# Optimization experiments

Measured on AMD Instinct MI355X. Metric: run time of the kernel, lower is better.

Reference implementation:

```python
import jax, jax.numpy as jnp
import numpy as np

N = 2_097_152  # total atoms
G = 32_768     # number of graphs (~64 atoms each)
EPS = 1e-4     # sign-detection threshold from the original code


def setup_inputs() -> dict:
    key = jax.random.key(0)
    k1, k2 = jax.random.split(key)
    pos = jax.random.normal(k1, (N, 3), dtype=jnp.float32) * 3.0
    batch = jnp.sort(jax.random.randint(k2, (N,), 0, G))
    return {"pos": pos, "batch": batch, "num_graphs": G}


def reference(pos, batch, num_graphs):
    n = pos.shape[0]
    dtype = pos.dtype

    # per-graph centroid (scatter_mean)
    counts = jax.ops.segment_sum(jnp.ones((n,), dtype), batch, num_segments=num_graphs)
    center = jax.ops.segment_sum(pos, batch, num_segments=num_graphs) / jnp.maximum(counts, 1.0)[:, None]
    pc = pos - center[batch]                      # [N,3] centered positions

    # per-atom inertia contribution: r^2 * I - p p^T, then scatter_add per graph
    r_sq = jnp.sum(pc * pc, axis=-1)              # [N]
    outer = jnp.einsum('ni,nj->nij', pc, pc)      # [N,3,3]
    I_atom = r_sq[:, None, None] * jnp.eye(3, dtype=dtype) - outer
    I_mol = jax.ops.segment_sum(I_atom, batch, num_segments=num_graphs)  # [G,3,3]

    L, Q = jnp.linalg.eigh(I_mol)                 # Q: [G,3,3], columns = principal axes

    # projections of centered positions onto the (pre-flip) eigenbasis.
    # NOTE: in the torch loop, p_proj is computed once before any sign flips, and
    # flipping column 0 does not affect p_proj[:,1], so axes 0 and 1 are independent.
    proj = jnp.einsum('ni,nij->nj', pc, Q[batch])  # [N,3]

    idx = jnp.arange(n)

    def axis_sign(a):
        # parallel "first atom (in original order) with |proj| > EPS" per graph
        qual = jnp.abs(proj[:, a]) > EPS
        key_idx = jnp.where(qual, idx, n)
        first = jax.ops.segment_min(key_idx, batch, num_segments=num_graphs)  # [G]
        found = first < n
        val = proj[jnp.minimum(first, n - 1), a]
        return jnp.where(found & (val < 0), -1.0, 1.0).astype(dtype)

    s0 = axis_sign(0)
    s1 = axis_sign(1)
    q0 = Q[:, :, 0] * s0[:, None]
    q1 = Q[:, :, 1] * s1[:, None]
    q2 = jnp.cross(q0, q1)  # enforce right-handed frame
    return jnp.stack([q0, q1, q2], axis=-1)       # [G,3,3]
```

## Files before the change

### kernel.cpp

```cpp
#include <hip/hip_runtime.h>
#include <math.h>

#define CANON_EPS 1e-4f
#define SUB 8
#define SUBMASK 0xFFu

__global__ void build_starts_kernel(const int* __restrict__ batch,
                                    int* __restrict__ starts, int n, int G) {
  int i = blockIdx.x * blockDim.x + threadIdx.x;
  if (i >= n) return;
  int b = batch[i];
  int bp = (i == 0) ? -1 : batch[i - 1];
  for (int g = bp + 1; g <= b; ++g) starts[g] = i;
  if (i == n - 1) {
    for (int g = b + 1; g <= G; ++g) starts[g] = n;
  }
}

__device__ __forceinline__ float red8(float v) {
  v += __shfl_xor(v, 1);
  v += __shfl_xor(v, 2);
  v += __shfl_xor(v, 4);
  return v;
}

__device__ __forceinline__ void jacobi3_f32(float a00, float a11, float a22,
                                            float a01, float a02, float a12,
                                            float Q[3][3]) {
  float A00 = a00, A11 = a11, A22 = a22;
  float A01 = a01, A02 = a02, A12 = a12;
  float Q00 = 1.f, Q01 = 0.f, Q02 = 0.f;
  float Q10 = 0.f, Q11 = 1.f, Q12 = 0.f;
  float Q20 = 0.f, Q21 = 0.f, Q22 = 1.f;

#define ROT(App, Aqq, Apq, Akp, Akq, Qrp0, Qrq0, Qrp1, Qrq1, Qrp2, Qrq2)     \
  {                                                                          \
    float apq = Apq;                                                         \
    float theta = (Aqq - App) / (2.0f * apq);                                \
    float t = copysignf(1.0f, theta) /                                       \
              (fabsf(theta) + sqrtf(1.0f + theta * theta));                  \
    t = (apq == 0.0f) ? 0.0f : t;                    \
    float c = 1.0f / sqrtf(1.0f + t * t);                                    \
    float s = t * c;                                                         \
    App = App - t * apq;                                                     \
    Aqq = Aqq + t * apq;                                                     \
    Apq = 0.0f;                                                              \
    float akp = Akp, akq = Akq;                                              \
    Akp = c * akp - s * akq;                                                 \
    Akq = s * akp + c * akq;                                                 \
    float r0p = Qrp0, r0q = Qrq0;                                            \
    Qrp0 = c * r0p - s * r0q;                                                \
    Qrq0 = s * r0p + c * r0q;                                                \
    float r1p = Qrp1, r1q = Qrq1;                                            \
    Qrp1 = c * r1p - s * r1q;                                                \
    Qrq1 = s * r1p + c * r1q;                                                \
    float r2p = Qrp2, r2q = Qrq2;                                            \
    Qrp2 = c * r2p - s * r2q;                                                \
    Qrq2 = s * r2p + c * r2q;                                                \
  }

#pragma unroll
  for (int sweep = 0; sweep < 5; ++sweep) {
    ROT(A00, A11, A01, A02, A12, Q00, Q01, Q10, Q11, Q20, Q21);
    ROT(A00, A22, A02, A01, A12, Q00, Q02, Q10, Q12, Q20, Q22);
    ROT(A11, A22, A12, A01, A02, Q01, Q02, Q11, Q12, Q21, Q22);
  }
#undef ROT

  float w0 = A00, w1 = A11, w2 = A22;
#define CSWAP(wa, wb, qa0, qb0, qa1, qb1, qa2, qb2)                          \
  {                                                                          \
    bool sw = (wb) < (wa);                                                   \
    float tw = wa; wa = sw ? wb : wa; wb = sw ? tw : wb;                     \
    float t0 = qa0; qa0 = sw ? qb0 : qa0; qb0 = sw ? t0 : qb0;               \
    float t1 = qa1; qa1 = sw ? qb1 : qa1; qb1 = sw ? t1 : qb1;               \
    float t2 = qa2; qa2 = sw ? qb2 : qa2; qb2 = sw ? t2 : qb2;               \
  }
  CSWAP(w0, w1, Q00, Q01, Q10, Q11, Q20, Q21);
  CSWAP(w1, w2, Q01, Q02, Q11, Q12, Q21, Q22);
  CSWAP(w0, w1, Q00, Q01, Q10, Q11, Q20, Q21);
#undef CSWAP

  Q[0][0] = Q00; Q[0][1] = Q01; Q[0][2] = Q02;
  Q[1][0] = Q10; Q[1][1] = Q11; Q[1][2] = Q12;
  Q[2][0] = Q20; Q[2][1] = Q21; Q[2][2] = Q22;
}

__global__ __launch_bounds__(256) void canon_kernel(
    const float* __restrict__ pos, const int* __restrict__ starts,
    float* __restrict__ out, int G) {
  int tid = (int)(blockIdx.x * (unsigned)blockDim.x + threadIdx.x);
  int gid = tid / SUB;
  int lane = (int)(threadIdx.x & 63u);
  int subw = lane / SUB;
  int sublane = lane & (SUB - 1);
  if (gid >= G) return;

  int s = starts[gid];
  int e = starts[gid + 1];
  int cnt = e - s;

  float sx = 0.f, sy = 0.f, sz = 0.f;
  float sxx = 0.f, syy = 0.f, szz = 0.f, sxy = 0.f, sxz = 0.f, syz = 0.f;
  for (int i = s + sublane; i < e; i += SUB) {
    float x = pos[3 * i + 0];
    float y = pos[3 * i + 1];
    float z = pos[3 * i + 2];
    sx += x; sy += y; sz += z;
    sxx = fmaf(x, x, sxx); syy = fmaf(y, y, syy); szz = fmaf(z, z, szz);
    sxy = fmaf(x, y, sxy); sxz = fmaf(x, z, sxz); syz = fmaf(y, z, syz);
  }
  sx = red8(sx); sy = red8(sy); sz = red8(sz);
  sxx = red8(sxx); syy = red8(syy); szz = red8(szz);
  sxy = red8(sxy); sxz = red8(sxz); syz = red8(syz);

  float fn = (float)(cnt > 0 ? cnt : 1);
  float inv = 1.0f / fn;
  float mx = sx * inv, my = sy * inv, mz = sz * inv;
  float Sxx = fmaf(-fn * mx, mx, sxx);
  float Syy = fmaf(-fn * my, my, syy);
  float Szz = fmaf(-fn * mz, mz, szz);
  float Sxy = fmaf(-fn * mx, my, sxy);
  float Sxz = fmaf(-fn * mx, mz, sxz);
  float Syz = fmaf(-fn * my, mz, syz);

  float ixx = Syy + Szz;
  float iyy = Sxx + Szz;
  float izz = Sxx + Syy;
  float ixy = -Sxy;
  float ixz = -Sxz;
  float iyz = -Syz;

  float Q[3][3];
  jacobi3_f32(ixx, iyy, izz, ixy, ixz, iyz, Q);

  float q00 = Q[0][0], q10 = Q[1][0], q20 = Q[2][0];
  float q01 = Q[0][1], q11 = Q[1][1], q21 = Q[2][1];

  bool found0 = false, found1 = false;
  float v0 = 0.f, v1 = 0.f;
  int it = 0;
  while (true) {
    int i = s + it * SUB + sublane;
    bool in = i < e;
    float p0 = 0.f, p1 = 0.f;
    if (in) {
      float x = pos[3 * i + 0] - mx;
      float y = pos[3 * i + 1] - my;
      float z = pos[3 * i + 2] - mz;
      p0 = x * q00 + y * q10 + z * q20;
      p1 = x * q01 + y * q11 + z * q21;
    }
    unsigned long long b0 = __ballot(in && (fabsf(p0) > CANON_EPS));
    unsigned long long b1 = __ballot(in && (fabsf(p1) > CANON_EPS));
    unsigned m0 = (unsigned)((b0 >> (subw * SUB)) & SUBMASK);
    unsigned m1 = (unsigned)((b1 >> (subw * SUB)) & SUBMASK);
    if (!found0 && m0) {
      int l = __ffs(m0) - 1;
      v0 = __shfl(p0, subw * SUB + l);
      found0 = true;
    }
    if (!found1 && m1) {
      int l = __ffs(m1) - 1;
      v1 = __shfl(p1, subw * SUB + l);
      found1 = true;
    }
    bool exhausted = (s + it * SUB) >= e;
    bool mydone = (found0 && found1) || exhausted;
    if (__all(mydone)) break;
    ++it;
  }
  float s0 = (found0 && v0 < 0.f) ? -1.f : 1.f;
  float s1 = (found1 && v1 < 0.f) ? -1.f : 1.f;

  if (sublane == 0) {
    float q0x = q00 * s0, q0y = q10 * s0, q0z = q20 * s0;
    float q1x = q01 * s1, q1y = q11 * s1, q1z = q21 * s1;
    float q2x = q0y * q1z - q0z * q1y;
    float q2y = q0z * q1x - q0x * q1z;
    float q2z = q0x * q1y - q0y * q1x;
    float* o = out + (size_t)gid * 9;
    o[0] = q0x; o[1] = q1x; o[2] = q2x;
    o[3] = q0y; o[4] = q1y; o[5] = q2y;
    o[6] = q0z; o[7] = q1z; o[8] = q2z;
  }
}

extern "C" void kernel_launch(void* const* d_in, const int* in_sizes, int n_in,
                              void* d_out, int out_size, void* d_ws, size_t ws_size,
                              hipStream_t stream) {
  const float* pos = (const float*)d_in[0];
  const int* batch = (const int*)d_in[1];
  float* out = (float*)d_out;

  int n = in_sizes[0] / 3;
  int G = out_size / 9;

  int* starts = (int*)d_ws;

  build_starts_kernel<<<(n + 255) / 256, 256, 0, stream>>>(batch, starts, n, G);

  int gper = 256 / SUB;
  int blocks = (G + gper - 1) / gper;
  canon_kernel<<<blocks, 256, 0, stream>>>(pos, starts, out, G);
}
```

Measured before the change: 26.12 us.

## Split moments reduction and eigen/sign pass into separate kernels

The fused per-graph kernel is split in two. The first kernel uses 16 lanes per graph to reduce the first and second moments and writes centroid and inertia terms to workspace in structure-of-arrays form. The second kernel runs one thread per graph, performing the Jacobi eigensolve and a serial scan for the first atom above the threshold, so the expensive eigensolve is no longer repeated redundantly across 8 lanes. The cost is an extra launch and workspace round trip, and the serial sign scan reads pos uncoalesced, though it usually stops after the first atom.

```diff
diff --git a/kernel.cpp b/kernel.cpp
--- a/kernel.cpp
+++ b/kernel.cpp
@@ -2,8 +2,7 @@
 #include <math.h>
 
 #define CANON_EPS 1e-4f
-#define SUB 8
-#define SUBMASK 0xFFu
+#define SUBA 16
 
 __global__ void build_starts_kernel(const int* __restrict__ batch,
                                     int* __restrict__ starts, int n, int G) {
@@ -17,11 +16,60 @@
   }
 }
 
-__device__ __forceinline__ float red8(float v) {
+__device__ __forceinline__ float red16(float v) {
   v += __shfl_xor(v, 1);
   v += __shfl_xor(v, 2);
   v += __shfl_xor(v, 4);
+  v += __shfl_xor(v, 8);
   return v;
+}
+
+__global__ __launch_bounds__(256) void moments_kernel(
+    const float* __restrict__ pos, const int* __restrict__ starts,
+    float* __restrict__ wsf, int G) {
+  int tid = (int)(blockIdx.x * (unsigned)blockDim.x + threadIdx.x);
+  int gid = tid / SUBA;
+  int sublane = tid & (SUBA - 1);
+  if (gid >= G) return;
+
+  int s = starts[gid];
+  int e = starts[gid + 1];
+  int cnt = e - s;
+
+  float sx = 0.f, sy = 0.f, sz = 0.f;
+  float sxx = 0.f, syy = 0.f, szz = 0.f, sxy = 0.f, sxz = 0.f, syz = 0.f;
+  for (int i = s + sublane; i < e; i += SUBA) {
+    float x = pos[3 * i + 0];
+    float y = pos[3 * i + 1];
+    float z = pos[3 * i + 2];
+    sx += x; sy += y; sz += z;
+    sxx = fmaf(x, x, sxx); syy = fmaf(y, y, syy); szz = fmaf(z, z, szz);
+    sxy = fmaf(x, y, sxy); sxz = fmaf(x, z, sxz); syz = fmaf(y, z, syz);
+  }
+  sx = red16(sx); sy = red16(sy); sz = red16(sz);
+  sxx = red16(sxx); syy = red16(syy); szz = red16(szz);
+  sxy = red16(sxy); sxz = red16(sxz); syz = red16(syz);
+
+  float fn = (float)(cnt > 0 ? cnt : 1);
+  float inv = 1.0f / fn;
+  float mx = sx * inv, my = sy * inv, mz = sz * inv;
+  float Sxx = fmaf(-fn * mx, mx, sxx);
+  float Syy = fmaf(-fn * my, my, syy);
+  float Szz = fmaf(-fn * mz, mz, szz);
+  float Sxy = fmaf(-fn * mx, my, sxy);
+  float Sxz = fmaf(-fn * mx, mz, sxz);
+  float Syz = fmaf(-fn * my, mz, syz);
+
+  float v = mx;
+  v = (sublane == 1) ? my : v;
+  v = (sublane == 2) ? mz : v;
+  v = (sublane == 3) ? (Syy + Szz) : v;
+  v = (sublane == 4) ? (Sxx + Szz) : v;
+  v = (sublane == 5) ? (Sxx + Syy) : v;
+  v = (sublane == 6) ? (-Sxy) : v;
+  v = (sublane == 7) ? (-Sxz) : v;
+  v = (sublane == 8) ? (-Syz) : v;
+  if (sublane < 9) wsf[sublane * G + gid] = v;
 }
 
 __device__ __forceinline__ void jacobi3_f32(float a00, float a11, float a22,
@@ -86,50 +134,21 @@
   Q[2][0] = Q20; Q[2][1] = Q21; Q[2][2] = Q22;
 }
 
-__global__ __launch_bounds__(256) void canon_kernel(
+__global__ __launch_bounds__(64) void eigen_kernel(
     const float* __restrict__ pos, const int* __restrict__ starts,
-    float* __restrict__ out, int G) {
-  int tid = (int)(blockIdx.x * (unsigned)blockDim.x + threadIdx.x);
-  int gid = tid / SUB;
-  int lane = (int)(threadIdx.x & 63u);
-  int subw = lane / SUB;
-  int sublane = lane & (SUB - 1);
-  if (gid >= G) return;
-
-  int s = starts[gid];
-  int e = starts[gid + 1];
-  int cnt = e - s;
-
-  float sx = 0.f, sy = 0.f, sz = 0.f;
-  float sxx = 0.f, syy = 0.f, szz = 0.f, sxy = 0.f, sxz = 0.f, syz = 0.f;
-  for (int i = s + sublane; i < e; i += SUB) {
-    float x = pos[3 * i + 0];
-    float y = pos[3 * i + 1];
-    float z = pos[3 * i + 2];
-    sx += x; sy += y; sz += z;
-    sxx = fmaf(x, x, sxx); syy = fmaf(y, y, syy); szz = fmaf(z, z, szz);
-    sxy = fmaf(x, y, sxy); sxz = fmaf(x, z, sxz); syz = fmaf(y, z, syz);
-  }
-  sx = red8(sx); sy = red8(sy); sz = red8(sz);
-  sxx = red8(sxx); syy = red8(syy); szz = red8(szz);
-  sxy = red8(sxy); sxz = red8(sxz); syz = red8(syz);
-
-  float fn = (float)(cnt > 0 ? cnt : 1);
-  float inv = 1.0f / fn;
-  float mx = sx * inv, my = sy * inv, mz = sz * inv;
-  float Sxx = fmaf(-fn * mx, mx, sxx);
-  float Syy = fmaf(-fn * my, my, syy);
-  float Szz = fmaf(-fn * mz, mz, szz);
-  float Sxy = fmaf(-fn * mx, my, sxy);
-  float Sxz = fmaf(-fn * mx, mz, sxz);
-  float Syz = fmaf(-fn * my, mz, syz);
-
-  float ixx = Syy + Szz;
-  float iyy = Sxx + Szz;
-  float izz = Sxx + Syy;
-  float ixy = -Sxy;
-  float ixz = -Sxz;
-  float iyz = -Syz;
+    const float* __restrict__ wsf, float* __restrict__ out, int G) {
+  int g = (int)(blockIdx.x * (unsigned)blockDim.x + threadIdx.x);
+  if (g >= G) return;
+
+  float cx  = wsf[0 * G + g];
+  float cy  = wsf[1 * G + g];
+  float cz  = wsf[2 * G + g];
+  float ixx = wsf[3 * G + g];
+  float iyy = wsf[4 * G + g];
+  float izz = wsf[5 * G + g];
+  float ixy = wsf[6 * G + g];
+  float ixz = wsf[7 * G + g];
+  float iyz = wsf[8 * G + g];
 
   float Q[3][3];
   jacobi3_f32(ixx, iyy, izz, ixy, ixz, iyz, Q);
@@ -137,53 +156,33 @@
   float q00 = Q[0][0], q10 = Q[1][0], q20 = Q[2][0];
   float q01 = Q[0][1], q11 = Q[1][1], q21 = Q[2][1];
 
+  int s = starts[g];
+  int e = starts[g + 1];
+
   bool found0 = false, found1 = false;
   float v0 = 0.f, v1 = 0.f;
-  int it = 0;
-  while (true) {
-    int i = s + it * SUB + sublane;
-    bool in = i < e;
-    float p0 = 0.f, p1 = 0.f;
-    if (in) {
-      float x = pos[3 * i + 0] - mx;
-      float y = pos[3 * i + 1] - my;
-      float z = pos[3 * i + 2] - mz;
-      p0 = x * q00 + y * q10 + z * q20;
-      p1 = x * q01 + y * q11 + z * q21;
-    }
-    unsigned long long b0 = __ballot(in && (fabsf(p0) > CANON_EPS));
-    unsigned long long b1 = __ballot(in && (fabsf(p1) > CANON_EPS));
-    unsigned m0 = (unsigned)((b0 >> (subw * SUB)) & SUBMASK);
-    unsigned m1 = (unsigned)((b1 >> (subw * SUB)) & SUBMASK);
-    if (!found0 && m0) {
-      int l = __ffs(m0) - 1;
-      v0 = __shfl(p0, subw * SUB + l);
-      found0 = true;
-    }
-    if (!found1 && m1) {
-      int l = __ffs(m1) - 1;
-      v1 = __shfl(p1, subw * SUB + l);
-      found1 = true;
-    }
-    bool exhausted = (s + it * SUB) >= e;
-    bool mydone = (found0 && found1) || exhausted;
-    if (__all(mydone)) break;
-    ++it;
+  for (int i = s; i < e; ++i) {
+    float x = pos[3 * i + 0] - cx;
+    float y = pos[3 * i + 1] - cy;
+    float z = pos[3 * i + 2] - cz;
+    float p0 = x * q00 + y * q10 + z * q20;
+    float p1 = x * q01 + y * q11 + z * q21;
+    if (!found0 && fabsf(p0) > CANON_EPS) { v0 = p0; found0 = true; }
+    if (!found1 && fabsf(p1) > CANON_EPS) { v1 = p1; found1 = true; }
+    if (found0 && found1) break;
   }
   float s0 = (found0 && v0 < 0.f) ? -1.f : 1.f;
   float s1 = (found1 && v1 < 0.f) ? -1.f : 1.f;
 
-  if (sublane == 0) {
-    float q0x = q00 * s0, q0y = q10 * s0, q0z = q20 * s0;
-    float q1x = q01 * s1, q1y = q11 * s1, q1z = q21 * s1;
-    float q2x = q0y * q1z - q0z * q1y;
-    float q2y = q0z * q1x - q0x * q1z;
-    float q2z = q0x * q1y - q0y * q1x;
-    float* o = out + (size_t)gid * 9;
-    o[0] = q0x; o[1] = q1x; o[2] = q2x;
-    o[3] = q0y; o[4] = q1y; o[5] = q2y;
-    o[6] = q0z; o[7] = q1z; o[8] = q2z;
-  }
+  float q0x = q00 * s0, q0y = q10 * s0, q0z = q20 * s0;
+  float q1x = q01 * s1, q1y = q11 * s1, q1z = q21 * s1;
+  float q2x = q0y * q1z - q0z * q1y;
+  float q2y = q0z * q1x - q0x * q1z;
+  float q2z = q0x * q1y - q0y * q1x;
+  float* o = out + (size_t)g * 9;
+  o[0] = q0x; o[1] = q1x; o[2] = q2x;
+  o[3] = q0y; o[4] = q1y; o[5] = q2y;
+  o[6] = q0z; o[7] = q1z; o[8] = q2z;
 }
 
 extern "C" void kernel_launch(void* const* d_in, const int* in_sizes, int n_in,
@@ -197,10 +196,12 @@
   int G = out_size / 9;
 
   int* starts = (int*)d_ws;
+  float* wsf = (float*)((char*)d_ws + ((size_t)(G + 1) * 4 + 255 & ~255ull));
 
   build_starts_kernel<<<(n + 255) / 256, 256, 0, stream>>>(batch, starts, n, G);
 
-  int gper = 256 / SUB;
-  int blocks = (G + gper - 1) / gper;
-  canon_kernel<<<blocks, 256, 0, stream>>>(pos, starts, out, G);
-}
+  int gperA = 256 / SUBA;
+  moments_kernel<<<(G + gperA - 1) / gperA, 256, 0, stream>>>(pos, starts, wsf, G);
+
+  eigen_kernel<<<(G + 63) / 64, 64, 0, stream>>>(pos, starts, wsf, out, G);
+}
```

Measured after the change: 23.68 us. 1.1x faster.
